# Kernel optimization log

Measured on AMD Instinct MI355X. Metric: run time of the kernel, lower is better.

## Reference

```python
import jax, jax.numpy as jnp
import numpy as np
import math

B, S, DIM = 4, 1024, 4096
N_HEADS, N_KV_HEADS = 32, 8
HEAD_DIM = DIM // N_HEADS  # 128
PAST = 1024
N_REP = N_HEADS // N_KV_HEADS


def _rope_freqs(seq_len, head_dim, theta=10000.0):
    inv = 1.0 / (theta ** (np.arange(0, head_dim, 2, dtype=np.float32) / head_dim))
    t = np.arange(seq_len, dtype=np.float32)
    ang = np.outer(t, inv)  # (S, head_dim//2)
    return jnp.asarray(np.cos(ang)), jnp.asarray(np.sin(ang))


def setup_inputs() -> dict:
    key = jax.random.key(0)
    ks = jax.random.split(key, 8)
    sc = 0.02
    x = jax.random.normal(ks[0], (B, S, DIM), dtype=jnp.float32)
    freqs_cos, freqs_sin = _rope_freqs(S, HEAD_DIM)
    cache_k = jax.random.normal(ks[1], (B, N_KV_HEADS, PAST, HEAD_DIM), dtype=jnp.float32)
    cache_v = jax.random.normal(ks[2], (B, N_KV_HEADS, PAST, HEAD_DIM), dtype=jnp.float32)
    wq = jax.random.normal(ks[3], (DIM, DIM), dtype=jnp.float32) * sc
    wk = jax.random.normal(ks[4], (N_KV_HEADS * HEAD_DIM, DIM), dtype=jnp.float32) * sc
    wv = jax.random.normal(ks[5], (N_KV_HEADS * HEAD_DIM, DIM), dtype=jnp.float32) * sc
    wo = jax.random.normal(ks[6], (DIM, DIM), dtype=jnp.float32) * sc
    return {"x": x, "freqs_cos": freqs_cos, "freqs_sin": freqs_sin,
            "cache_k": cache_k, "cache_v": cache_v,
            "wq": wq, "wk": wk, "wv": wv, "wo": wo}


def _apply_rotary(x, cos, sin):
    # x: (b, h, s, d); cos/sin: (s, d//2) broadcast to (1, 1, s, d//2)
    xr = x.reshape(*x.shape[:-1], -1, 2)
    x_r, x_i = xr[..., 0], xr[..., 1]
    cos = cos[None, None, :, :]
    sin = sin[None, None, :, :]
    out_r = x_r * cos - x_i * sin
    out_i = x_r * sin + x_i * cos
    return jnp.stack([out_r, out_i], axis=-1).reshape(x.shape)


def reference(x, freqs_cos, freqs_sin, cache_k, cache_v, wq, wk, wv, wo):
    bsz, seqlen, _ = x.shape
    xq = x @ wq.T  # (b, s, n_heads*hd)
    xk = x @ wk.T  # (b, s, n_kv*hd)
    xv = x @ wv.T
    xq = xq.reshape(bsz, seqlen, N_HEADS, HEAD_DIM).transpose(0, 2, 1, 3)
    xk = xk.reshape(bsz, seqlen, N_KV_HEADS, HEAD_DIM).transpose(0, 2, 1, 3)
    xv = xv.reshape(bsz, seqlen, N_KV_HEADS, HEAD_DIM).transpose(0, 2, 1, 3)
    xq = _apply_rotary(xq, freqs_cos, freqs_sin)
    xk = _apply_rotary(xk, freqs_cos, freqs_sin)
    keys = jnp.concatenate([cache_k, xk], axis=2)    # (b, kvh, past+s, hd)
    values = jnp.concatenate([cache_v, xv], axis=2)
    keys = jnp.repeat(keys, N_REP, axis=1)            # (b, h, kv, hd)
    values = jnp.repeat(values, N_REP, axis=1)
    scores = jnp.einsum('bhsd,bhkd->bhsk', xq, keys) / math.sqrt(HEAD_DIM)
    scores = jax.nn.softmax(scores, axis=-1)          # no mask (inference path)
    out = jnp.einsum('bhsk,bhkd->bhsd', scores, values)
    out = out.transpose(0, 2, 1, 3).reshape(bsz, seqlen, -1)
    return out @ wo.T
```

## Files before the change

### kernel.cpp

```cpp
#include <hip/hip_runtime.h>
#include <hip/hip_bf16.h>

using bf16 = __hip_bfloat16;
typedef __attribute__((ext_vector_type(4))) float f4;
typedef __attribute__((ext_vector_type(16))) float f16v;
typedef __attribute__((ext_vector_type(8))) short s8v;
typedef __attribute__((ext_vector_type(4))) short s4v;
typedef __attribute__((ext_vector_type(4))) unsigned int u4v;
typedef unsigned int u32;

__device__ __forceinline__ short f2bf(float x) {
  bf16 h = __float2bfloat16(x);
  return *reinterpret_cast<short*>(&h);
}

__device__ __forceinline__ u32 pkbf(float lo, float hi) {
  return (u32)(unsigned short)f2bf(lo) | ((u32)(unsigned short)f2bf(hi) << 16);
}

__device__ __forceinline__ void gload16(const bf16* g, bf16* l) {
  __builtin_amdgcn_global_load_lds(
      (const __attribute__((address_space(1))) u32*)g,
      (__attribute__((address_space(3))) u32*)l, 16, 0, 0);
}

__device__ __forceinline__ void swp32(u32& a, u32& b, int h) {
#if __has_builtin(__builtin_amdgcn_permlane32_swap)
  typedef __attribute__((ext_vector_type(2))) int i2v;
  i2v r = __builtin_amdgcn_permlane32_swap((int)a, (int)b, false, false);
  a = (u32)r.x;
  b = (u32)r.y;
#else
  u32 as = (u32)__shfl_xor((int)a, 32), bs = (u32)__shfl_xor((int)b, 32);
  u32 an = h ? bs : a, bn = h ? b : as;
  a = an;
  b = bn;
#endif
}

__device__ __forceinline__ float xhalf_max(float x) {
#if __has_builtin(__builtin_amdgcn_permlane32_swap)
  typedef __attribute__((ext_vector_type(2))) int i2v;
  i2v r = __builtin_amdgcn_permlane32_swap(__float_as_int(x), __float_as_int(x),
                                           false, false);
  return fmaxf(__int_as_float(r.x), __int_as_float(r.y));
#else
  return fmaxf(x, __shfl_xor(x, 32));
#endif
}
__device__ __forceinline__ float xhalf_sum(float x) {
#if __has_builtin(__builtin_amdgcn_permlane32_swap)
  typedef __attribute__((ext_vector_type(2))) int i2v;
  i2v r = __builtin_amdgcn_permlane32_swap(__float_as_int(x), __float_as_int(x),
                                           false, false);
  return __int_as_float(r.x) + __int_as_float(r.y);
#else
  return x + __shfl_xor(x, 32);
#endif
}

__global__ __launch_bounds__(256) void cvt_bf16(const float* __restrict__ src,
                                                bf16* __restrict__ dst) {
  size_t e = ((size_t)blockIdx.x * 256 + threadIdx.x) << 3;
  f4 a = *(const f4*)(src + e);
  f4 b = *(const f4*)(src + e + 4);
  s8v r = { f2bf(a[0]), f2bf(a[1]), f2bf(a[2]), f2bf(a[3]),
            f2bf(b[0]), f2bf(b[1]), f2bf(b[2]), f2bf(b[3]) };
  *(s8v*)(dst + e) = r;
}

__global__ __launch_bounds__(256) void cvt_cache_k(const float* __restrict__ src,
                                                   bf16* __restrict__ dst) {
  size_t e = ((size_t)blockIdx.x * 256 + threadIdx.x) << 2;
  f4 v = *(const f4*)(src + e);
  unsigned d = (unsigned)(e & 127u), p = (unsigned)((e >> 7) & 1023u), bk = (unsigned)(e >> 17);
  s4v r = { f2bf(v[0]), f2bf(v[1]), f2bf(v[2]), f2bf(v[3]) };
  *(s4v*)(dst + (((size_t)bk * 2048 + p) << 7) + d) = r;
}

__global__ __launch_bounds__(256) void cvt_cache_v(const float* __restrict__ src,
                                                   bf16* __restrict__ dst) {
  size_t e = ((size_t)blockIdx.x * 256 + threadIdx.x) << 2;
  unsigned p = (unsigned)(e & 1023u), d = (unsigned)((e >> 10) & 127u), bk = (unsigned)(e >> 17);
  const float* s = src + (((size_t)bk * 1024 + p) << 7) + d;
  s4v r = { f2bf(s[0]), f2bf(s[128]), f2bf(s[256]), f2bf(s[384]) };
  *(s4v*)(dst + (((size_t)bk * 128 + d) << 11) + p) = r;
}

__global__ __launch_bounds__(256) void rope_kernel(bf16* __restrict__ buf,
                                                   const float* __restrict__ fc,
                                                   const float* __restrict__ fs,
                                                   int sstride, int soff) {
  size_t t = (size_t)blockIdx.x * 256 + threadIdx.x;
  unsigned ip = (unsigned)(t & 63u);
  unsigned s  = (unsigned)((t >> 6) & 1023u);
  unsigned hh = (unsigned)(t >> 16);
  size_t base = ((size_t)hh * sstride + soff + s) * 128 + 2 * ip;
  unsigned u = *(unsigned*)(buf + base);
  float xr = __uint_as_float(u << 16);
  float xi = __uint_as_float(u & 0xffff0000u);
  float c = fc[s * 64 + ip], sn = fs[s * 64 + ip];
  unsigned short r0 = (unsigned short)f2bf(xr * c - xi * sn);
  unsigned short r1 = (unsigned short)f2bf(xr * sn + xi * c);
  *(unsigned*)(buf + base) = (unsigned)r0 | ((unsigned)r1 << 16);
}

#define MODE_Q   0
#define MODE_OUT 1

#define PHASE_TAIL(AC, BC, KS, MH)                                           \
  {                                                                          \
    s8v af[4], bv[4];                                                        \
    const int cofs = ((((KS) * 4) | g) ^ fx) << 3;                           \
    _Pragma("unroll") for (int mi = 0; mi < 4; ++mi)                         \
        af[mi] = *(const s8v*)&(AC)[aRowBase + ((MH)*4 + mi) * 1024 + cofs]; \
    _Pragma("unroll") for (int ni = 0; ni < 4; ++ni)                         \
        bv[ni] = *(const s8v*)&(BC)[bRowBase + ni * 1024 + cofs];            \
    __builtin_amdgcn_s_barrier();                                            \
    asm volatile("s_waitcnt lgkmcnt(0)" ::: "memory");                       \
    __builtin_amdgcn_s_setprio(1);                                           \
    _Pragma("unroll") for (int mi = 0; mi < 4; ++mi)                         \
      _Pragma("unroll") for (int ni = 0; ni < 4; ++ni)                       \
          acc[(MH)*4 + mi][ni] = __builtin_amdgcn_mfma_f32_16x16x32_bf16(    \
              af[mi], bv[ni], acc[(MH)*4 + mi][ni], 0, 0, 0);                \
    __builtin_amdgcn_s_setprio(0);                                           \
    __builtin_amdgcn_s_barrier();                                            \
  }

#define PHASE_HEAD(AC, BC)                                                   \
  {                                                                          \
    __builtin_amdgcn_s_barrier();                                            \
    s8v af[4], bv[4];                                                        \
    const int cofs = (g ^ fx) << 3;                                          \
    _Pragma("unroll") for (int mi = 0; mi < 4; ++mi)                         \
        af[mi] = *(const s8v*)&(AC)[aRowBase + mi * 1024 + cofs];            \
    _Pragma("unroll") for (int ni = 0; ni < 4; ++ni)                         \
        bv[ni] = *(const s8v*)&(BC)[bRowBase + ni * 1024 + cofs];            \
    asm volatile("s_waitcnt lgkmcnt(0)" ::: "memory");                       \
    __builtin_amdgcn_s_setprio(1);                                           \
    _Pragma("unroll") for (int mi = 0; mi < 4; ++mi)                         \
      _Pragma("unroll") for (int ni = 0; ni < 4; ++ni)                       \
          acc[mi][ni] = __builtin_amdgcn_mfma_f32_16x16x32_bf16(             \
              af[mi], bv[ni], acc[mi][ni], 0, 0, 0);                         \
    __builtin_amdgcn_s_setprio(0);                                           \
    __builtin_amdgcn_s_barrier();                                            \
  }

#define KTILE(AC, BC, PA, PB, NA, NB, PF)                                    \
  {                                                                          \
    if (PF) { gload16((NA), (PA)); gload16((NA) + rstep, (PA) + 4096); }     \
    if (PF) asm volatile("s_waitcnt vmcnt(2)" ::: "memory");                 \
    else    asm volatile("s_waitcnt vmcnt(0)" ::: "memory");                 \
    PHASE_HEAD(AC, BC)                                                       \
    if (PF) { gload16((NA) + 2 * rstep, (PA) + 8192);                        \
              gload16((NA) + 3 * rstep, (PA) + 12288); }                     \
    PHASE_TAIL(AC, BC, 0, 1)                                                 \
    if (PF) { gload16((NB), (PB)); gload16((NB) + rstep, (PB) + 4096); }     \
    PHASE_TAIL(AC, BC, 1, 0)                                                 \
    if (PF) { gload16((NB) + 2 * rstep, (PB) + 8192);                        \
              gload16((NB) + 3 * rstep, (PB) + 12288); }                     \
    PHASE_TAIL(AC, BC, 1, 1)                                                 \
  }

template <int MODE>
__global__ __launch_bounds__(512, 2) void gemm256(const bf16* __restrict__ A,
                                                  const bf16* __restrict__ B,
                                                  void* __restrict__ o1,
                                                  int K, float scale) {
  extern __shared__ bf16 smem[];
  bf16* A0 = smem;
  bf16* A1 = smem + 16384;
  bf16* B0 = smem + 32768;
  bf16* B1 = smem + 49152;

  const int tid = threadIdx.x;
  const int lane = tid & 63;
  const int wid = tid >> 6;
  const int wm = wid >> 2, wn = wid & 3;
  const int fr = lane & 15;
  const int g = lane >> 4;
  const int rg = g << 2;
  const int fx = lane & 7;

  const int gy = gridDim.y;
  int lin = blockIdx.y * gridDim.x + blockIdx.x;
  const int qq = (gridDim.x * gy) >> 3;
  lin = (lin & 7) * qq + (lin >> 3);
  const int bm = lin / gy;
  const int bn = lin % gy;

  const int r0 = tid >> 3;
  const int sc = (tid & 7) ^ (r0 & 7);
  const bf16* aptr = A + (size_t)(bm * 256 + r0) * K + sc * 8;
  const bf16* bptr = B + (size_t)(bn * 256 + r0) * K + sc * 8;
  const size_t rstep = (size_t)64 * K;
  const int wofs = (tid & 448) << 3;
  bf16* pA0 = A0 + wofs; bf16* pA1 = A1 + wofs;
  bf16* pB0 = B0 + wofs; bf16* pB1 = B1 + wofs;

  const int aRowBase = (wm * 128 + fr) * 64;
  const int bRowBase = (wn * 64 + fr) * 64;

  f4 acc[8][4] = {};

#pragma unroll
  for (int i = 0; i < 4; ++i) gload16(aptr + i * rstep, pA0 + i * 4096);
#pragma unroll
  for (int i = 0; i < 4; ++i) gload16(bptr + i * rstep, pB0 + i * 4096);

  const int nk = K >> 6;
  for (int kt = 0; kt < nk; kt += 2) {
    const bf16* na = aptr + (kt + 1) * 64;
    const bf16* nb = bptr + (kt + 1) * 64;
    KTILE(A0, B0, pA1, pB1, na, nb, true)
    const bool pf2 = (kt + 2 < nk);
    const bf16* na2 = aptr + (kt + 2) * 64;
    const bf16* nb2 = bptr + (kt + 2) * 64;
    KTILE(A1, B1, pA0, pB0, na2, nb2, pf2)
  }

#pragma unroll
  for (int m = 0; m < 8; ++m) {
    const int grow0 = bm * 256 + wm * 128 + m * 16 + rg;
    const int b = grow0 >> 10, s0 = grow0 & 1023;
#pragma unroll
    for (int n = 0; n < 4; ++n) {
      const int gcol = bn * 256 + wn * 64 + n * 16 + fr;
      if constexpr (MODE == MODE_OUT) {
#pragma unroll
        for (int j = 0; j < 4; ++j)
          ((float*)o1)[(size_t)(grow0 + j) * 4096 + gcol] = acc[m][n][j];
      } else {
        const int h = gcol >> 7, d = gcol & 127;
#pragma unroll
        for (int j = 0; j < 4; ++j)
          ((bf16*)o1)[((((size_t)b * 32 + h) << 10) + s0 + j) * 128 + d] =
              __float2bfloat16(acc[m][n][j] * scale);
      }
    }
  }
}

#define PH128(AC, BC, KS, OPEN)                                              \
  {                                                                          \
    if (OPEN) __builtin_amdgcn_s_barrier();                                  \
    s8v af[4], bv[4];                                                        \
    const int cofs = ((((KS) * 4) | g) ^ fx) << 3;                           \
    _Pragma("unroll") for (int mi = 0; mi < 4; ++mi)                         \
        af[mi] = *(const s8v*)&(AC)[aRowBase + mi * 1024 + cofs];            \
    _Pragma("unroll") for (int ni = 0; ni < 4; ++ni)                         \
        bv[ni] = *(const s8v*)&(BC)[bRowBase + ni * 1024 + cofs];            \
    if (!(OPEN)) __builtin_amdgcn_s_barrier();                               \
    asm volatile("s_waitcnt lgkmcnt(0)" ::: "memory");                       \
    __builtin_amdgcn_s_setprio(1);                                           \
    _Pragma("unroll") for (int mi = 0; mi < 4; ++mi)                         \
      _Pragma("unroll") for (int ni = 0; ni < 4; ++ni)                       \
          acc[mi][ni] = __builtin_amdgcn_mfma_f32_16x16x32_bf16(             \
              af[mi], bv[ni], acc[mi][ni], 0, 0, 0);                         \
    __builtin_amdgcn_s_setprio(0);                                           \
    __builtin_amdgcn_s_barrier();                                            \
  }

#define KTILE128(AC, BC, PA, PB, NA, NB, PF)                                 \
  {                                                                          \
    if (PF) { gload16((NB), (PB)); gload16((NB) + rstep, (PB) + 4096); }     \
    if (PF) asm volatile("s_waitcnt vmcnt(2)" ::: "memory");                 \
    else    asm volatile("s_waitcnt vmcnt(0)" ::: "memory");                 \
    PH128(AC, BC, 0, true)                                                   \
    if (PF) { gload16((NB) + 2 * rstep, (PB) + 8192);                        \
              gload16((NB) + 3 * rstep, (PB) + 12288);                       \
              gload16((NA), (PA)); gload16((NA) + rstep, (PA) + 4096); }     \
    PH128(AC, BC, 1, false)                                                  \
  }

__global__ __launch_bounds__(512, 2) void gemm128kv(const bf16* __restrict__ A,
                                                    const bf16* __restrict__ B,
                                                    bf16* __restrict__ kout,
                                                    bf16* __restrict__ vout,
                                                    int K) {
  extern __shared__ bf16 smem[];
  bf16* A0 = smem;
  bf16* A1 = smem + 8192;
  bf16* B0 = smem + 16384;
  bf16* B1 = smem + 32768;

  const int tid = threadIdx.x;
  const int lane = tid & 63;
  const int wid = tid >> 6;
  const int wm = wid >> 2, wn = wid & 3;
  const int fr = lane & 15;
  const int g = lane >> 4;
  const int rg = g << 2;
  const int fx = lane & 7;

  const int gy = gridDim.y;
  int lin = blockIdx.y * gridDim.x + blockIdx.x;
  const int qq = (gridDim.x * gy) >> 3;
  lin = (lin & 7) * qq + (lin >> 3);
  const int bm = lin / gy;
  const int bn = lin % gy;

  const int r0 = tid >> 3;
  const int sc = (tid & 7) ^ (r0 & 7);
  const bf16* aptr = A + (size_t)(bm * 128 + r0) * K + sc * 8;
  const bf16* bptr = B + (size_t)(bn * 256 + r0) * K + sc * 8;
  const size_t rstep = (size_t)64 * K;
  const int wofs = (tid & 448) << 3;
  bf16* pA0 = A0 + wofs; bf16* pA1 = A1 + wofs;
  bf16* pB0 = B0 + wofs; bf16* pB1 = B1 + wofs;

  const int aRowBase = (wm * 64 + fr) * 64;
  const int bRowBase = (wn * 64 + fr) * 64;

  f4 acc[4][4] = {};

  gload16(aptr, pA0); gload16(aptr + rstep, pA0 + 4096);
#pragma unroll
  for (int i = 0; i < 4; ++i) gload16(bptr + i * rstep, pB0 + i * 4096);

  const int nk = K >> 6;
  for (int kt = 0; kt < nk; kt += 2) {
    const bf16* na = aptr + (kt + 1) * 64;
    const bf16* nb = bptr + (kt + 1) * 64;
    KTILE128(A0, B0, pA1, pB1, na, nb, true)
    const bool pf2 = (kt + 2 < nk);
    const bf16* na2 = aptr + (kt + 2) * 64;
    const bf16* nb2 = bptr + (kt + 2) * 64;
    KTILE128(A1, B1, pA0, pB0, na2, nb2, pf2)
  }

#pragma unroll
  for (int m = 0; m < 4; ++m) {
    const int grow0 = bm * 128 + wm * 64 + m * 16 + rg;
    const int b = grow0 >> 10, s0 = grow0 & 1023;
#pragma unroll
    for (int n = 0; n < 4; ++n) {
      const int gcol = bn * 256 + wn * 64 + n * 16 + fr;
      if (gcol < 1024) {
        const int hv = gcol >> 7, d = gcol & 127;
#pragma unroll
        for (int j = 0; j < 4; ++j)
          kout[(((size_t)b * 8 + hv) * 2048 + 1024 + s0 + j) * 128 + d] =
              __float2bfloat16(acc[m][n][j]);
      } else {
        const int c = gcol - 1024, hv = c >> 7, d = c & 127;
        s4v r = { f2bf(acc[m][n][0]), f2bf(acc[m][n][1]),
                  f2bf(acc[m][n][2]), f2bf(acc[m][n][3]) };
        *(s4v*)(vout + (((size_t)b * 8 + hv) * 128 + d) * 2048 + 1024 + s0) = r;
      }
    }
  }
}

__global__ __launch_bounds__(512) void attn_kernel(const bf16* __restrict__ Q,
                                                   const bf16* __restrict__ Kf,
                                                   const bf16* __restrict__ Vt,
                                                   bf16* __restrict__ O) {
  __shared__ alignas(16) bf16 Kls[2][8192];
  __shared__ alignas(16) bf16 Vls[2][8192];

  const int tid = threadIdx.x;
  const int lane = tid & 63;
  const int w = tid >> 6;
  const int h = lane >> 5;
  const int q31 = lane & 31;
  const int rx = q31 & 7;

  int lin = blockIdx.y * 4 + blockIdx.x;
  lin = (lin & 7) * 64 + (lin >> 3);
  const int qb = lin & 3;
  const int hrem = (lin >> 2) & 3;
  const int pair = lin >> 4;
  const int b = pair >> 3, kv = pair & 7;
  const int hd = kv * 4 + hrem;

  const size_t qbase = (((size_t)b * 32 + hd) << 10) * 128;
  const size_t kbase = (((size_t)b * 8 + kv) * 2048) * 128;
  const size_t vbase = (((size_t)b * 8 + kv) * 128) * 2048;

  const int qrow = qb * 256 + w * 32 + q31;
  s8v qf[8];
#pragma unroll
  for (int c = 0; c < 8; ++c)
    qf[c] = *(const s8v*)&Q[qbase + (size_t)qrow * 128 + c * 16 + h * 8];

  const int sr = tid >> 3;
  const int swz8 = (((tid & 7) ^ (sr & 7)) << 3);
  const int wbase = w * 512;

  f16v oacc[4] = {};
  float mrun = -3e38f, lrun = 0.f;

  auto stage = [&](int kb, int bufi) {
    const bf16* ksrc = Kf + kbase + (size_t)(kb * 64 + sr) * 128 + swz8;
    gload16(ksrc,      &Kls[bufi][wbase]);
    gload16(ksrc + 64, &Kls[bufi][4096 + wbase]);
    const bf16* vsrc = Vt + vbase + (size_t)sr * 2048 + kb * 64 + swz8;
    gload16(vsrc,                      &Vls[bufi][wbase]);
    gload16(vsrc + (size_t)64 * 2048,  &Vls[bufi][4096 + wbase]);
  };

  stage(0, 0);
  asm volatile("s_waitcnt vmcnt(0)" ::: "memory");
  __syncthreads();

  for (int kb = 0; kb < 32; ++kb) {
    const int bufi = kb & 1;
    if (kb + 1 < 32) stage(kb + 1, bufi ^ 1);

    const bf16* KB = Kls[bufi];
    const bf16* VB = Vls[bufi];

    f16v sac[2] = {};
    __builtin_amdgcn_s_setprio(1);
#pragma unroll
    for (int c = 0; c < 8; ++c) {
      const int cc = 2 * c + h;
      const int cof = (cc >> 3) * 4096 + (((cc & 7) ^ rx) << 3);
      s8v k0 = *(const s8v*)&KB[cof + q31 * 64];
      s8v k1 = *(const s8v*)&KB[cof + (32 + q31) * 64];
      sac[0] = __builtin_amdgcn_mfma_f32_32x32x16_bf16(k0, qf[c], sac[0], 0, 0, 0);
      sac[1] = __builtin_amdgcn_mfma_f32_32x32x16_bf16(k1, qf[c], sac[1], 0, 0, 0);
    }
    __builtin_amdgcn_s_setprio(0);

    float pm = -3e38f;
#pragma unroll
    for (int r = 0; r < 16; ++r) {
      pm = fmaxf(pm, sac[0][r]);
      pm = fmaxf(pm, sac[1][r]);
    }
    pm = xhalf_max(pm);

    const bool skip = __all(pm <= mrun + 8.0f);
    if (!skip) {
      const float mnew = fmaxf(mrun, pm);
      const float corr = exp2f(mrun - mnew);
      mrun = mnew;
      lrun *= corr;
#pragma unroll
      for (int m = 0; m < 4; ++m)
#pragma unroll
        for (int r = 0; r < 16; ++r) oacc[m][r] *= corr;
    }
    float ls = 0.f;
#pragma unroll
    for (int s = 0; s < 2; ++s)
#pragma unroll
      for (int r = 0; r < 16; ++r) {
        const float p = exp2f(sac[s][r] - mrun);
        sac[s][r] = p;
        ls += p;
      }
    lrun += xhalf_sum(ls);

    s8v F[4];
#pragma unroll
    for (int s = 0; s < 2; ++s) {
      u32 W[8];
#pragma unroll
      for (int t = 0; t < 8; ++t) W[t] = pkbf(sac[s][2 * t], sac[s][2 * t + 1]);
      swp32(W[0], W[2], h); swp32(W[1], W[3], h);
      swp32(W[4], W[6], h); swp32(W[5], W[7], h);
      union { u32 u[4]; s8v v; } f0, f1;
      f0.u[0] = W[0]; f0.u[1] = W[1]; f0.u[2] = W[2]; f0.u[3] = W[3];
      f1.u[0] = W[4]; f1.u[1] = W[5]; f1.u[2] = W[6]; f1.u[3] = W[7];
      F[s * 2] = f0.v;
      F[s * 2 + 1] = f1.v;
    }

    __builtin_amdgcn_s_setprio(1);
#pragma unroll
    for (int ksg = 0; ksg < 4; ++ksg) {
      const int cc2 = 2 * ksg + h;
      const int vof = ((cc2 ^ rx) << 3);
#pragma unroll
      for (int m = 0; m < 4; ++m) {
        s8v vf = *(const s8v*)&VB[(m * 32 + q31) * 64 + vof];
        oacc[m] = __builtin_amdgcn_mfma_f32_32x32x16_bf16(vf, F[ksg], oacc[m], 0, 0, 0);
      }
    }
    __builtin_amdgcn_s_setprio(0);

    asm volatile("s_waitcnt vmcnt(0)" ::: "memory");
    __syncthreads();
  }

  const float inv = 1.f / lrun;
  bf16* orow = O + ((size_t)b * 1024 + qrow) * 4096 + hd * 128;
#pragma unroll
  for (int m = 0; m < 4; ++m)
#pragma unroll
    for (int r = 0; r < 16; r += 2) {
      const int d = m * 32 + (r & 3) + 8 * (r >> 2) + 4 * h;
      *(u32*)&orow[d] = pkbf(oacc[m][r] * inv, oacc[m][r + 1] * inv);
    }
}

extern "C" void kernel_launch(void* const* d_in, const int* in_sizes, int n_in,
                              void* d_out, int out_size, void* d_ws, size_t ws_size,
                              hipStream_t stream) {
  const float* x  = (const float*)d_in[0];
  const float* fc = (const float*)d_in[1];
  const float* fs = (const float*)d_in[2];
  const float* ck = (const float*)d_in[3];
  const float* cv = (const float*)d_in[4];
  const float* wq = (const float*)d_in[5];
  const float* wk = (const float*)d_in[6];
  const float* wv = (const float*)d_in[7];
  const float* wo = (const float*)d_in[8];
  float* out = (float*)d_out;

  char* ws = (char*)d_ws;
  bf16* qr    = (bf16*)(ws);
  bf16* kfull = (bf16*)(ws + (32u << 20));
  bf16* vt    = (bf16*)(ws + (48u << 20));
  bf16* xb    = (bf16*)(ws + (64u << 20));
  bf16* attn  = xb;
  bf16* wqb   = (bf16*)(ws + (96u << 20));
  bf16* wob   = wqb;
  bf16* wkvb  = (bf16*)(ws + (128u << 20));

  hipFuncSetAttribute(reinterpret_cast<const void*>(&gemm256<MODE_Q>),
                      hipFuncAttributeMaxDynamicSharedMemorySize, 131072);
  hipFuncSetAttribute(reinterpret_cast<const void*>(&gemm256<MODE_OUT>),
                      hipFuncAttributeMaxDynamicSharedMemorySize, 131072);
  hipFuncSetAttribute(reinterpret_cast<const void*>(&gemm128kv),
                      hipFuncAttributeMaxDynamicSharedMemorySize, 98304);

  cvt_bf16<<<8192, 256, 0, stream>>>(x, xb);
  cvt_bf16<<<8192, 256, 0, stream>>>(wq, wqb);
  cvt_bf16<<<2048, 256, 0, stream>>>(wk, wkvb);
  cvt_bf16<<<2048, 256, 0, stream>>>(wv, wkvb + 4194304);
  cvt_cache_k<<<4096, 256, 0, stream>>>(ck, kfull);
  cvt_cache_v<<<4096, 256, 0, stream>>>(cv, vt);

  gemm256<MODE_Q><<<dim3(16, 16), 512, 131072, stream>>>(
      xb, wqb, qr, 4096, 0.1275174198520337f);
  gemm128kv<<<dim3(32, 8), 512, 98304, stream>>>(xb, wkvb, kfull, vt, 4096);

  cvt_bf16<<<8192, 256, 0, stream>>>(wo, wob);

  rope_kernel<<<32768, 256, 0, stream>>>(qr, fc, fs, 1024, 0);
  rope_kernel<<<8192, 256, 0, stream>>>(kfull, fc, fs, 2048, 1024);

  attn_kernel<<<dim3(4, 128), 512, 0, stream>>>(qr, kfull, vt, attn);

  gemm256<MODE_OUT><<<dim3(16, 16), 512, 131072, stream>>>(
      attn, wob, out, 4096, 1.0f);
}
```

Measured before the change: 619.9 us.

## Permute K rows to drop lane swaps and compute softmax row sums via MFMA

The K-tile rows read for the QK^T MFMA are permuted so the score accumulator layout directly matches the B-operand layout of the PV MFMA, which removes the permlane32 swaps used to repack probabilities. The running softmax denominator is now accumulated by an extra MFMA against a ones matrix instead of scalar adds plus a cross-half reduction. This trades VALU and cross-lane work for four extra MFMAs per tile and a 16-register accumulator. The denominator is now summed from bf16-rounded probabilities, which matches the values used for the numerator.

```diff
diff --git a/kernel.cpp b/kernel.cpp
--- a/kernel.cpp
+++ b/kernel.cpp
@@ -22,41 +22,6 @@
   __builtin_amdgcn_global_load_lds(
       (const __attribute__((address_space(1))) u32*)g,
       (__attribute__((address_space(3))) u32*)l, 16, 0, 0);
-}
-
-__device__ __forceinline__ void swp32(u32& a, u32& b, int h) {
-#if __has_builtin(__builtin_amdgcn_permlane32_swap)
-  typedef __attribute__((ext_vector_type(2))) int i2v;
-  i2v r = __builtin_amdgcn_permlane32_swap((int)a, (int)b, false, false);
-  a = (u32)r.x;
-  b = (u32)r.y;
-#else
-  u32 as = (u32)__shfl_xor((int)a, 32), bs = (u32)__shfl_xor((int)b, 32);
-  u32 an = h ? bs : a, bn = h ? b : as;
-  a = an;
-  b = bn;
-#endif
-}
-
-__device__ __forceinline__ float xhalf_max(float x) {
-#if __has_builtin(__builtin_amdgcn_permlane32_swap)
-  typedef __attribute__((ext_vector_type(2))) int i2v;
-  i2v r = __builtin_amdgcn_permlane32_swap(__float_as_int(x), __float_as_int(x),
-                                           false, false);
-  return fmaxf(__int_as_float(r.x), __int_as_float(r.y));
-#else
-  return fmaxf(x, __shfl_xor(x, 32));
-#endif
-}
-__device__ __forceinline__ float xhalf_sum(float x) {
-#if __has_builtin(__builtin_amdgcn_permlane32_swap)
-  typedef __attribute__((ext_vector_type(2))) int i2v;
-  i2v r = __builtin_amdgcn_permlane32_swap(__float_as_int(x), __float_as_int(x),
-                                           false, false);
-  return __int_as_float(r.x) + __int_as_float(r.y);
-#else
-  return x + __shfl_xor(x, 32);
-#endif
 }
 
 __global__ __launch_bounds__(256) void cvt_bf16(const float* __restrict__ src,
@@ -364,7 +329,9 @@
   const int w = tid >> 6;
   const int h = lane >> 5;
   const int q31 = lane & 31;
-  const int rx = q31 & 7;
+  const int pq = (q31 & 19) | ((q31 & 4) << 1) | ((q31 & 8) >> 1);
+  const int rxK = pq & 7;
+  const int rxV = q31 & 7;
 
   int lin = blockIdx.y * 4 + blockIdx.x;
   lin = (lin & 7) * 64 + (lin >> 3);
@@ -384,12 +351,18 @@
   for (int c = 0; c < 8; ++c)
     qf[c] = *(const s8v*)&Q[qbase + (size_t)qrow * 128 + c * 16 + h * 8];
 
+  union { u32 u[4]; s8v v; } onesu;
+#pragma unroll
+  for (int i = 0; i < 4; ++i) onesu.u[i] = 0x3F803F80u;
+  const s8v onesA = onesu.v;
+
   const int sr = tid >> 3;
   const int swz8 = (((tid & 7) ^ (sr & 7)) << 3);
   const int wbase = w * 512;
 
   f16v oacc[4] = {};
-  float mrun = -3e38f, lrun = 0.f;
+  f16v lacc = {};
+  float mrun = -3e38f;
 
   auto stage = [&](int kb, int bufi) {
     const bf16* ksrc = Kf + kbase + (size_t)(kb * 64 + sr) * 128 + swz8;
@@ -416,9 +389,9 @@
 #pragma unroll
     for (int c = 0; c < 8; ++c) {
       const int cc = 2 * c + h;
-      const int cof = (cc >> 3) * 4096 + (((cc & 7) ^ rx) << 3);
-      s8v k0 = *(const s8v*)&KB[cof + q31 * 64];
-      s8v k1 = *(const s8v*)&KB[cof + (32 + q31) * 64];
+      const int cof = (cc >> 3) * 4096 + (((cc & 7) ^ rxK) << 3);
+      s8v k0 = *(const s8v*)&KB[cof + pq * 64];
+      s8v k1 = *(const s8v*)&KB[cof + (32 + pq) * 64];
       sac[0] = __builtin_amdgcn_mfma_f32_32x32x16_bf16(k0, qf[c], sac[0], 0, 0, 0);
       sac[1] = __builtin_amdgcn_mfma_f32_32x32x16_bf16(k1, qf[c], sac[1], 0, 0, 0);
     }
@@ -430,55 +403,49 @@
       pm = fmaxf(pm, sac[0][r]);
       pm = fmaxf(pm, sac[1][r]);
     }
-    pm = xhalf_max(pm);
+    pm = fmaxf(pm, __shfl_xor(pm, 32));
 
     const bool skip = __all(pm <= mrun + 8.0f);
     if (!skip) {
       const float mnew = fmaxf(mrun, pm);
       const float corr = exp2f(mrun - mnew);
       mrun = mnew;
-      lrun *= corr;
+#pragma unroll
+      for (int r = 0; r < 16; ++r) lacc[r] *= corr;
 #pragma unroll
       for (int m = 0; m < 4; ++m)
 #pragma unroll
         for (int r = 0; r < 16; ++r) oacc[m][r] *= corr;
     }
-    float ls = 0.f;
 #pragma unroll
     for (int s = 0; s < 2; ++s)
 #pragma unroll
-      for (int r = 0; r < 16; ++r) {
-        const float p = exp2f(sac[s][r] - mrun);
-        sac[s][r] = p;
-        ls += p;
-      }
-    lrun += xhalf_sum(ls);
+      for (int r = 0; r < 16; ++r)
+        sac[s][r] = exp2f(sac[s][r] - mrun);
 
     s8v F[4];
 #pragma unroll
-    for (int s = 0; s < 2; ++s) {
-      u32 W[8];
-#pragma unroll
-      for (int t = 0; t < 8; ++t) W[t] = pkbf(sac[s][2 * t], sac[s][2 * t + 1]);
-      swp32(W[0], W[2], h); swp32(W[1], W[3], h);
-      swp32(W[4], W[6], h); swp32(W[5], W[7], h);
-      union { u32 u[4]; s8v v; } f0, f1;
-      f0.u[0] = W[0]; f0.u[1] = W[1]; f0.u[2] = W[2]; f0.u[3] = W[3];
-      f1.u[0] = W[4]; f1.u[1] = W[5]; f1.u[2] = W[6]; f1.u[3] = W[7];
-      F[s * 2] = f0.v;
-      F[s * 2 + 1] = f1.v;
+    for (int ksg = 0; ksg < 4; ++ksg) {
+      const int s = ksg >> 1;
+      const int u8 = (ksg & 1) << 3;
+      union { u32 u[4]; s8v v; } fu;
+#pragma unroll
+      for (int t = 0; t < 4; ++t)
+        fu.u[t] = pkbf(sac[s][u8 + 2 * t], sac[s][u8 + 2 * t + 1]);
+      F[ksg] = fu.v;
     }
 
     __builtin_amdgcn_s_setprio(1);
 #pragma unroll
     for (int ksg = 0; ksg < 4; ++ksg) {
       const int cc2 = 2 * ksg + h;
-      const int vof = ((cc2 ^ rx) << 3);
+      const int vof = ((cc2 ^ rxV) << 3);
 #pragma unroll
       for (int m = 0; m < 4; ++m) {
         s8v vf = *(const s8v*)&VB[(m * 32 + q31) * 64 + vof];
         oacc[m] = __builtin_amdgcn_mfma_f32_32x32x16_bf16(vf, F[ksg], oacc[m], 0, 0, 0);
       }
+      lacc = __builtin_amdgcn_mfma_f32_32x32x16_bf16(onesA, F[ksg], lacc, 0, 0, 0);
     }
     __builtin_amdgcn_s_setprio(0);
 
@@ -486,7 +453,7 @@
     __syncthreads();
   }
 
-  const float inv = 1.f / lrun;
+  const float inv = 1.f / lacc[0];
   bf16* orow = O + ((size_t)b * 1024 + qrow) * 4096 + hd * 128;
 #pragma unroll
   for (int m = 0; m < 4; ++m)
```

Result: no change. 618.6 us (-0.2%).
